# Optimization experiments

Measured on AMD Instinct MI355X. Metric: run time of the kernel, lower is better.

Reference implementation:

```python
import jax, jax.numpy as jnp
import numpy as np
from jax import lax

# SLAYER neuron / simulation constants (from netParams)
THETA = 10.0       # spike threshold
TAU_SR = 10.0      # synaptic (PSP) time constant
TAU_REF = 1.0      # refractory time constant
SCALE_REF = 2.0    # refractory scale
TAU_RHO = 1.0      # surrogate-gradient width (unused in fwd)
K_PSP = 32         # truncation length of SRM alpha kernel
K_REF = 16         # truncation length of refractory kernel

_t = np.arange(K_PSP, dtype=np.float64)
PSP_KERN = jnp.asarray((_t / TAU_SR) * np.exp(1.0 - _t / TAU_SR), jnp.float32)  # [K_PSP]
_tr = np.arange(1, K_REF + 1, dtype=np.float64)
REF_KERN = jnp.asarray(-SCALE_REF * THETA * (_tr / TAU_REF) * np.exp(1.0 - _tr / TAU_REF), jnp.float32)  # [K_REF]


def psp(x):
    """Causal temporal FIR filter with SRM alpha kernel; x: [..., T]."""
    sh = x.shape
    T = sh[-1]
    flat = x.reshape(-1, 1, T)                       # [B*, 1, T]
    k = PSP_KERN[::-1][None, None, :]                # correlation kernel (reversed)
    y = lax.conv_general_dilated(flat, k, (1,), [(K_PSP - 1, 0)])
    return y.reshape(sh)


def spike(u):
    """Threshold with refractory feedback, sequential over time. u: [..., T]."""
    uT = jnp.moveaxis(u, -1, 0)                      # [T, ...]
    buf0 = jnp.zeros(u.shape[:-1] + (K_REF,), u.dtype)

    def step(buf, ut):
        v = ut + buf[..., 0]
        s = (v >= THETA).astype(u.dtype)
        buf = jnp.concatenate([buf[..., 1:], jnp.zeros_like(buf[..., :1])], -1)
        buf = buf + s[..., None] * REF_KERN
        return buf, s

    _, sT = lax.scan(step, buf0, uT)
    return jnp.moveaxis(sT, 0, -1)


def conv_t(x, w, stride, pad):
    """2D conv applied independently per timestep. x: [N,C,H,W,T], w: [Co,C,kh,kw]."""
    N, C, H, W, T = x.shape
    xt = jnp.moveaxis(x, -1, 1).reshape(N * T, C, H, W)
    y = lax.conv_general_dilated(xt, w, (stride, stride), [(pad, pad), (pad, pad)])
    Co, Ho, Wo = y.shape[1], y.shape[2], y.shape[3]
    return jnp.moveaxis(y.reshape(N, T, Co, Ho, Wo), 1, -1)


def pool_t(x):
    """SLAYER sum-pool 2x2/s2 with weight 1.1*theta/kernel_area. x: [N,C,H,W,T]."""
    s = lax.reduce_window(x, np.float32(0.0), lax.add, (1, 1, 2, 2, 1), (1, 1, 2, 2, 1), 'VALID')
    return s * np.float32(1.1 * THETA / 4.0)


def setup_inputs() -> dict:
    key = jax.random.key(0)
    ks = jax.random.split(key, 5)
    spikeInput = (jax.random.uniform(ks[0], (4, 2, 256, 256, 50)) < 0.02).astype(jnp.float32)
    w1 = jax.random.normal(ks[1], (8, 2, 5, 5), jnp.float32) * 2.0
    w2 = jax.random.normal(ks[2], (16, 8, 3, 3), jnp.float32) * 1.5
    w3 = jax.random.normal(ks[3], (32, 16, 3, 3), jnp.float32) * 1.5
    w_fc = jax.random.normal(ks[4], (2, 32, 8, 8), jnp.float32) * 0.3
    return {"spikeInput": spikeInput, "w1": w1, "w2": w2, "w3": w3, "w_fc": w_fc}


def reference(spikeInput, w1, w2, w3, w_fc):
    x = spike(conv_t(psp(spikeInput), w1, 2, 1))   # [4,8,127,127,50]
    x = spike(pool_t(psp(x)))                      # [4,8,63,63,50]
    x = spike(conv_t(psp(x), w2, 2, 1))            # [4,16,32,32,50]
    x = spike(pool_t(psp(x)))                      # [4,16,16,16,50]
    x = spike(conv_t(psp(x), w3, 2, 1))            # [4,32,8,8,50]
    u = psp(x)
    out = jnp.einsum('ochw,nchwt->not', w_fc, u)   # dense over (C,H,W)
    return spike(out[:, :, None, None, :])         # [4,2,1,1,50]
```

## Files before the change

### kernel.cpp

```cpp
#include <hip/hip_runtime.h>
#include <cmath>

struct K32 { float k[32]; };
struct K16 { float k[16]; };

#define THETA 10.0f

__global__ __launch_bounds__(128)
void psp_kernel(const float* __restrict__ in, float* __restrict__ out,
                int nrows, K32 pk) {
  __shared__ __align__(16) float lds[64 * 50];
  const int rowBase = blockIdx.x * 64;
  const int tid = threadIdx.x;
  const int vr = min(64, nrows - rowBase);
  const int n4 = (vr * 50) >> 2;
  const float4* g4 = (const float4*)(in + (size_t)rowBase * 50);
  for (int i = tid; i < n4; i += 128) *(float4*)(&lds[4 * i]) = g4[i];
  __syncthreads();
  const int r = tid & 63;
  const int part = tid >> 6;
  const bool act = r < vr;
  float x[50];
  if (act) {
    if (part == 0) {
#pragma unroll
      for (int t = 0; t < 25; ++t) x[t] = lds[r * 50 + t];
    } else {
#pragma unroll
      for (int t = 0; t < 50; ++t) x[t] = lds[r * 50 + t];
    }
  }
  __syncthreads();
  if (act) {
    if (part == 0) {
#pragma unroll
      for (int t = 0; t < 25; ++t) {
        float a = 0.f;
#pragma unroll
        for (int k = 31; k >= 0; --k)
          if (t - k >= 0) a += x[t - k] * pk.k[k];
        lds[r * 50 + t] = a;
      }
    } else {
#pragma unroll
      for (int t = 25; t < 50; ++t) {
        float a = 0.f;
#pragma unroll
        for (int k = 31; k >= 0; --k)
          if (t - k >= 0) a += x[t - k] * pk.k[k];
        lds[r * 50 + t] = a;
      }
    }
  }
  __syncthreads();
  float4* o4 = (float4*)(out + (size_t)rowBase * 50);
  for (int i = tid; i < n4; i += 128) o4[i] = *(const float4*)(&lds[4 * i]);
}

template <int CIN, int COUT, int KK, int HIN, int WIN, int S1H, int S1W,
          int S2H, int S2W>
__global__ __launch_bounds__(256)
void conv_pps_kernel(const float* __restrict__ x, const float* __restrict__ w,
                     float* __restrict__ s2out, K32 pk, K16 rk) {
  constexpr int WT = 4;
  constexpr int SW = 8;
  constexpr int XR = 2 * (WT - 1) + KK;
  constexpr int GROUPS = (S1W + SW - 1) / SW;
  constexpr int NROW = COUT * 2 * SW;
  __shared__ float lds[NROW * 51];
  const int tid = threadIdx.x;
  const int wave = tid >> 6;
  const int lane = tid & 63;
  const int group = blockIdx.x % GROUPS;
  const int rest = blockIdx.x / GROUPS;
  const int hop = rest % S2H;
  const int n = rest / S2H;
  const int ho_off = wave & 1;
  const int wo_half = wave >> 1;
  const int ho = 2 * hop + ho_off;
  const int wo0 = group * SW + wo_half * WT;
  const int tt = lane < 50 ? lane : 49;

  float acc[COUT][WT] = {};
  for (int c = 0; c < CIN; ++c) {
#pragma unroll
    for (int kh = 0; kh < KK; ++kh) {
      const int hi = 2 * ho + kh - 1;
      if ((unsigned)hi >= (unsigned)HIN) continue;
      float xr[XR];
#pragma unroll
      for (int i = 0; i < XR; ++i) {
        const int wi = 2 * wo0 - 1 + i;
        xr[i] = ((unsigned)wi < (unsigned)WIN)
                    ? x[(((size_t)(n * CIN + c) * HIN + hi) * WIN + wi) * 50 + tt]
                    : 0.f;
      }
#pragma unroll
      for (int co = 0; co < COUT; ++co)
#pragma unroll
        for (int kw = 0; kw < KK; ++kw) {
          const float wv = w[((co * CIN + c) * KK + kh) * KK + kw];
#pragma unroll
          for (int wl = 0; wl < WT; ++wl)
            acc[co][wl] += xr[2 * wl + kw] * wv;
        }
    }
  }
  if (lane < 50) {
#pragma unroll
    for (int co = 0; co < COUT; ++co)
#pragma unroll
      for (int wl = 0; wl < WT; ++wl)
        lds[((co * 2 + ho_off) * SW + wo_half * WT + wl) * 51 + lane] = acc[co][wl];
  }
  __syncthreads();
  if (tid < NROW) {
    const int wol = tid & (SW - 1);
    if (group * SW + wol < S1W) {
      float buf[16];
#pragma unroll
      for (int j = 0; j < 16; ++j) buf[j] = 0.f;
#pragma unroll
      for (int t = 0; t < 50; ++t) {
        float v = lds[tid * 51 + t] + buf[t & 15];
        buf[t & 15] = 0.f;
        float sp = 0.f;
        if (v >= THETA) {
          sp = 1.f;
#pragma unroll
          for (int j = 0; j < 16; ++j) buf[(t + 1 + j) & 15] += rk.k[j];
        }
        lds[tid * 51 + t] = sp;
      }
    }
  }
  __syncthreads();
  {
    const int r = tid & (NROW - 1);
    const int part = tid >> 7;
    const int wol = r & (SW - 1);
    const bool act = (group * SW + wol) < S1W;
    float xs[50];
    if (act) {
      if (part == 0) {
#pragma unroll
        for (int t = 0; t < 25; ++t) xs[t] = lds[r * 51 + t];
      } else {
#pragma unroll
        for (int t = 0; t < 50; ++t) xs[t] = lds[r * 51 + t];
      }
    }
    __syncthreads();
    if (act) {
      if (part == 0) {
#pragma unroll
        for (int t = 0; t < 25; ++t) {
          float a = 0.f;
#pragma unroll
          for (int k = 31; k >= 0; --k)
            if (t - k >= 0) a += xs[t - k] * pk.k[k];
          lds[r * 51 + t] = a;
        }
      } else {
#pragma unroll
        for (int t = 25; t < 50; ++t) {
          float a = 0.f;
#pragma unroll
          for (int k = 31; k >= 0; --k)
            if (t - k >= 0) a += xs[t - k] * pk.k[k];
          lds[r * 51 + t] = a;
        }
      }
    }
  }
  __syncthreads();
  if (tid < COUT * (SW / 2)) {
    const int co = tid / (SW / 2);
    const int wpl = tid % (SW / 2);
    const int wop = group * (SW / 2) + wpl;
    if (wop < S2W) {
      const int r00 = (co * 16 + 2 * wpl) * 51;
      const int r01 = (co * 16 + 2 * wpl + 1) * 51;
      const int r10 = (co * 16 + 8 + 2 * wpl) * 51;
      const int r11 = (co * 16 + 8 + 2 * wpl + 1) * 51;
      float* orow = s2out + (((size_t)(n * COUT + co) * S2H + hop) * S2W + wop) * 50;
      float buf[16];
#pragma unroll
      for (int j = 0; j < 16; ++j) buf[j] = 0.f;
      float prev = 0.f;
#pragma unroll
      for (int t = 0; t < 50; ++t) {
        const float u0 = (((lds[r00 + t] + lds[r01 + t]) + lds[r10 + t]) + lds[r11 + t]) * 2.75f;
        float v = u0 + buf[t & 15];
        buf[t & 15] = 0.f;
        float sp = 0.f;
        if (v >= THETA) {
          sp = 1.f;
#pragma unroll
          for (int j = 0; j < 16; ++j) buf[(t + 1 + j) & 15] += rk.k[j];
        }
        if (t & 1) *(float2*)(orow + t - 1) = make_float2(prev, sp);
        else prev = sp;
      }
    }
  }
}

template <int CIN, int COUT, int KK, int WT, int HIN, int WIN, int HOUT, int WOUT>
__global__ __launch_bounds__(256)
void conv_spike_kernel(const float* __restrict__ x, const float* __restrict__ w,
                       float* __restrict__ s, K16 rk) {
  constexpr int XR = 2 * (WT - 1) + KK;
  constexpr int TW = 4 * WT;
  constexpr int GROUPS = (WOUT + TW - 1) / TW;
  __shared__ float lds[COUT * TW * 51];
  const int tid = threadIdx.x;
  const int wave = tid >> 6;
  const int lane = tid & 63;
  const int group = blockIdx.x % GROUPS;
  const int rest = blockIdx.x / GROUPS;
  const int ho = rest % HOUT;
  const int n = rest / HOUT;
  const int wo0 = group * TW + wave * WT;
  const int tt = lane < 50 ? lane : 49;

  float acc[COUT][WT] = {};
  for (int c = 0; c < CIN; ++c) {
#pragma unroll
    for (int kh = 0; kh < KK; ++kh) {
      const int hi = 2 * ho + kh - 1;
      if ((unsigned)hi >= (unsigned)HIN) continue;
      float xr[XR];
#pragma unroll
      for (int i = 0; i < XR; ++i) {
        const int wi = 2 * wo0 - 1 + i;
        xr[i] = ((unsigned)wi < (unsigned)WIN)
                    ? x[(((size_t)(n * CIN + c) * HIN + hi) * WIN + wi) * 50 + tt]
                    : 0.f;
      }
#pragma unroll
      for (int co = 0; co < COUT; ++co)
#pragma unroll
        for (int kw = 0; kw < KK; ++kw) {
          const float wv = w[((co * CIN + c) * KK + kh) * KK + kw];
#pragma unroll
          for (int wl = 0; wl < WT; ++wl)
            acc[co][wl] += xr[2 * wl + kw] * wv;
        }
    }
  }

  if (lane < 50) {
#pragma unroll
    for (int co = 0; co < COUT; ++co)
#pragma unroll
      for (int wl = 0; wl < WT; ++wl)
        lds[(co * TW + wave * WT + wl) * 51 + lane] = acc[co][wl];
  }
  __syncthreads();
  if (tid < COUT * TW) {
    const int co = tid / TW;
    const int wol = tid - co * TW;
    const int wo = group * TW + wol;
    if (wo < WOUT) {
      float* orow = s + (((size_t)(n * COUT + co) * HOUT + ho) * WOUT + wo) * 50;
      float buf[16];
#pragma unroll
      for (int j = 0; j < 16; ++j) buf[j] = 0.f;
      float prev = 0.f;
#pragma unroll
      for (int t = 0; t < 50; ++t) {
        float v = lds[tid * 51 + t] + buf[t & 15];
        buf[t & 15] = 0.f;
        float sp = 0.f;
        if (v >= THETA) {
          sp = 1.f;
#pragma unroll
          for (int j = 0; j < 16; ++j) buf[(t + 1 + j) & 15] += rk.k[j];
        }
        if (t & 1) *(float2*)(orow + t - 1) = make_float2(prev, sp);
        else prev = sp;
      }
    }
  }
}

__global__ __launch_bounds__(128)
void pps_kernel(const float* __restrict__ in, float* __restrict__ out,
                int Hin, int Win, int Hout, int Wout, int nseg,
                K32 pk, K16 rk) {
  __shared__ __align__(16) float lds[80 * 50];
  const int tid = threadIdx.x;
  const int seg = blockIdx.x % nseg;
  const int rest = blockIdx.x / nseg;
  const int ho = rest % Hout;
  const int nc = rest / Hout;
  const int wbase = seg * 32;
  const int nw = min(32, 2 * Wout - wbase);
  const int nwo = nw >> 1;
  const int span = nw * 50;
  const float* b0 = in + ((size_t)(nc * Hin + 2 * ho) * Win + wbase) * 50;
  const float* b1 = b0 + (size_t)Win * 50;
  const int n2 = span >> 1;
  for (int i = tid; i < n2; i += 128) {
    *(float2*)(&lds[2 * i]) = *(const float2*)(b0 + 2 * i);
    *(float2*)(&lds[span + 2 * i]) = *(const float2*)(b1 + 2 * i);
  }
  __syncthreads();
  const int r = tid & 63;
  const int part = tid >> 6;
  const bool act = r < 2 * nw;
  float x[50];
  if (act) {
    if (part == 0) {
#pragma unroll
      for (int t = 0; t < 25; ++t) x[t] = lds[r * 50 + t];
    } else {
#pragma unroll
      for (int t = 0; t < 50; ++t) x[t] = lds[r * 50 + t];
    }
  }
  __syncthreads();
  if (act) {
    if (part == 0) {
#pragma unroll
      for (int t = 0; t < 25; ++t) {
        float a = 0.f;
#pragma unroll
        for (int k = 31; k >= 0; --k)
          if (t - k >= 0) a += x[t - k] * pk.k[k];
        lds[r * 50 + t] = a;
      }
    } else {
#pragma unroll
      for (int t = 25; t < 50; ++t) {
        float a = 0.f;
#pragma unroll
        for (int k = 31; k >= 0; --k)
          if (t - k >= 0) a += x[t - k] * pk.k[k];
        lds[r * 50 + t] = a;
      }
    }
  }
  __syncthreads();
  if (tid < nwo) {
    float buf[16];
#pragma unroll
    for (int j = 0; j < 16; ++j) buf[j] = 0.f;
    const int r00 = (2 * tid) * 50, r01 = (2 * tid + 1) * 50;
    const int r10 = (nw + 2 * tid) * 50, r11 = (nw + 2 * tid + 1) * 50;
    const int ro = (2 * nw + tid) * 50;
#pragma unroll
    for (int t = 0; t < 50; ++t) {
      const float u0 = (((lds[r00 + t] + lds[r01 + t]) + lds[r10 + t]) + lds[r11 + t]) * 2.75f;
      float v = u0 + buf[t & 15];
      buf[t & 15] = 0.f;
      float sp = 0.f;
      if (v >= THETA) {
        sp = 1.f;
#pragma unroll
        for (int j = 0; j < 16; ++j) buf[(t + 1 + j) & 15] += rk.k[j];
      }
      lds[ro + t] = sp;
    }
  }
  __syncthreads();
  float* ob = out + ((size_t)(nc * Hout + ho) * Wout + seg * 16) * 50;
  const int base = 2 * nw * 50;
  for (int i = tid; i < nwo * 25; i += 128)
    *(float2*)(ob + 2 * i) = *(const float2*)(&lds[base + 2 * i]);
}

__global__ __launch_bounds__(512)
void fc_spike_kernel(const float* __restrict__ w, const float* __restrict__ u,
                     float* __restrict__ out, K16 rk) {
  __shared__ float lds[8 * 51];
  const int tid = threadIdx.x;
  const int wave = tid >> 6, lane = tid & 63;
  const int o = wave & 1, n = wave >> 1;
  const int tt = lane < 50 ? lane : 49;
  const float* wrow = w + (size_t)o * 2048;
  const float* ub = u + (size_t)n * 2048 * 50;
  float acc = 0.f;
#pragma unroll 32
  for (int i = 0; i < 2048; ++i) acc += wrow[i] * ub[(size_t)i * 50 + tt];
  if (lane < 50) lds[wave * 51 + lane] = acc;
  __syncthreads();
  if (tid < 8) {
    float buf[16];
#pragma unroll
    for (int j = 0; j < 16; ++j) buf[j] = 0.f;
#pragma unroll
    for (int t = 0; t < 50; ++t) {
      float v = lds[tid * 51 + t] + buf[t & 15];
      buf[t & 15] = 0.f;
      float sp = 0.f;
      if (v >= THETA) {
        sp = 1.f;
#pragma unroll
        for (int j = 0; j < 16; ++j) buf[(t + 1 + j) & 15] += rk.k[j];
      }
      out[tid * 50 + t] = sp;
    }
  }
}

extern "C" void kernel_launch(void* const* d_in, const int* in_sizes, int n_in,
                              void* d_out, int out_size, void* d_ws, size_t ws_size,
                              hipStream_t stream) {
  const float* xin = (const float*)d_in[0];
  const float* w1  = (const float*)d_in[1];
  const float* w2  = (const float*)d_in[2];
  const float* w3  = (const float*)d_in[3];
  const float* wfc = (const float*)d_in[4];
  float* out = (float*)d_out;

  float* R0 = (float*)d_ws;
  float* R1 = R0 + 26214400;

  K32 pk;
  for (int k = 0; k < 32; ++k)
    pk.k[k] = (float)(((double)k / 10.0) * exp(1.0 - (double)k / 10.0));
  K16 rk;
  for (int j = 0; j < 16; ++j) {
    const double tr = (double)(j + 1);
    rk.k[j] = (float)(-2.0 * 10.0 * tr * exp(1.0 - tr));
  }

  psp_kernel<<<8192, 128, 0, stream>>>(xin, R0, 524288, pk);
  conv_pps_kernel<2, 8, 5, 256, 256, 127, 127, 63, 63>
      <<<4 * 63 * 16, 256, 0, stream>>>(R0, w1, R1, pk, rk);
  psp_kernel<<<1985, 128, 0, stream>>>(R1, R0, 127008, pk);
  conv_spike_kernel<8, 16, 3, 1, 63, 63, 32, 32>
      <<<4 * 32 * 8, 256, 0, stream>>>(R0, w2, R1, rk);
  pps_kernel<<<4 * 16 * 16, 128, 0, stream>>>(R1, R0, 32, 32, 16, 16, 1, pk, rk);
  psp_kernel<<<256, 128, 0, stream>>>(R0, R1, 16384, pk);
  conv_spike_kernel<16, 32, 3, 1, 16, 16, 8, 8>
      <<<4 * 8 * 2, 256, 0, stream>>>(R1, w3, R0, rk);
  psp_kernel<<<128, 128, 0, stream>>>(R0, R1, 8192, pk);
  fc_spike_kernel<<<1, 512, 0, stream>>>(wfc, R1, out, rk);
}
```

Baseline: 505.6 us.

## Commute PSP filter past linear conv, pool and FC stages and fuse into them

The temporal PSP filter is linear and acts per pixel, so it commutes with the per-timestep spatial convolutions, sum-pooling and the dense FC layer. Each PSP is therefore applied after the spatial op, inside the conv, pool and FC kernels, and all standalone psp_kernel launches are removed. This drops several full global-memory round trips, including the large filtered copy of the input, and cuts the launch count. In return each fused kernel does extra in-LDS FIR work, sometimes on more rows than before. The changed float summation order can flip spikes that sit right at the threshold.

```diff
diff --git a/kernel.cpp b/kernel.cpp
--- a/kernel.cpp
+++ b/kernel.cpp
@@ -5,57 +5,6 @@
 struct K16 { float k[16]; };
 
 #define THETA 10.0f
-
-__global__ __launch_bounds__(128)
-void psp_kernel(const float* __restrict__ in, float* __restrict__ out,
-                int nrows, K32 pk) {
-  __shared__ __align__(16) float lds[64 * 50];
-  const int rowBase = blockIdx.x * 64;
-  const int tid = threadIdx.x;
-  const int vr = min(64, nrows - rowBase);
-  const int n4 = (vr * 50) >> 2;
-  const float4* g4 = (const float4*)(in + (size_t)rowBase * 50);
-  for (int i = tid; i < n4; i += 128) *(float4*)(&lds[4 * i]) = g4[i];
-  __syncthreads();
-  const int r = tid & 63;
-  const int part = tid >> 6;
-  const bool act = r < vr;
-  float x[50];
-  if (act) {
-    if (part == 0) {
-#pragma unroll
-      for (int t = 0; t < 25; ++t) x[t] = lds[r * 50 + t];
-    } else {
-#pragma unroll
-      for (int t = 0; t < 50; ++t) x[t] = lds[r * 50 + t];
-    }
-  }
-  __syncthreads();
-  if (act) {
-    if (part == 0) {
-#pragma unroll
-      for (int t = 0; t < 25; ++t) {
-        float a = 0.f;
-#pragma unroll
-        for (int k = 31; k >= 0; --k)
-          if (t - k >= 0) a += x[t - k] * pk.k[k];
-        lds[r * 50 + t] = a;
-      }
-    } else {
-#pragma unroll
-      for (int t = 25; t < 50; ++t) {
-        float a = 0.f;
-#pragma unroll
-        for (int k = 31; k >= 0; --k)
-          if (t - k >= 0) a += x[t - k] * pk.k[k];
-        lds[r * 50 + t] = a;
-      }
-    }
-  }
-  __syncthreads();
-  float4* o4 = (float4*)(out + (size_t)rowBase * 50);
-  for (int i = tid; i < n4; i += 128) o4[i] = *(const float4*)(&lds[4 * i]);
-}
 
 template <int CIN, int COUT, int KK, int HIN, int WIN, int S1H, int S1W,
           int S2H, int S2W>
@@ -114,6 +63,45 @@
         lds[((co * 2 + ho_off) * SW + wo_half * WT + wl) * 51 + lane] = acc[co][wl];
   }
   __syncthreads();
+  {
+    const int r = tid & (NROW - 1);
+    const int part = tid >> 7;
+    const int wol = r & (SW - 1);
+    const bool act = (group * SW + wol) < S1W;
+    float xs[50];
+    if (act) {
+      if (part == 0) {
+#pragma unroll
+        for (int t = 0; t < 25; ++t) xs[t] = lds[r * 51 + t];
+      } else {
+#pragma unroll
+        for (int t = 0; t < 50; ++t) xs[t] = lds[r * 51 + t];
+      }
+    }
+    __syncthreads();
+    if (act) {
+      if (part == 0) {
+#pragma unroll
+        for (int t = 0; t < 25; ++t) {
+          float a = 0.f;
+#pragma unroll
+          for (int k = 31; k >= 0; --k)
+            if (t - k >= 0) a += xs[t - k] * pk.k[k];
+          lds[r * 51 + t] = a;
+        }
+      } else {
+#pragma unroll
+        for (int t = 25; t < 50; ++t) {
+          float a = 0.f;
+#pragma unroll
+          for (int k = 31; k >= 0; --k)
+            if (t - k >= 0) a += xs[t - k] * pk.k[k];
+          lds[r * 51 + t] = a;
+        }
+      }
+    }
+  }
+  __syncthreads();
   if (tid < NROW) {
     const int wol = tid & (SW - 1);
     if (group * SW + wol < S1W) {
@@ -136,18 +124,25 @@
   }
   __syncthreads();
   {
-    const int r = tid & (NROW - 1);
-    const int part = tid >> 7;
-    const int wol = r & (SW - 1);
-    const bool act = (group * SW + wol) < S1W;
+    const int r = tid & 31;
+    const int part = tid >> 5;
+    const int co = r >> 2;
+    const int wpl = r & 3;
+    const bool act = (part < 2) && (group * (SW / 2) + wpl < S2W);
+    const int r00 = (co * 16 + 2 * wpl) * 51;
+    const int r01 = r00 + 51;
+    const int r10 = (co * 16 + 8 + 2 * wpl) * 51;
+    const int r11 = r10 + 51;
     float xs[50];
     if (act) {
       if (part == 0) {
 #pragma unroll
-        for (int t = 0; t < 25; ++t) xs[t] = lds[r * 51 + t];
-      } else {
-#pragma unroll
-        for (int t = 0; t < 50; ++t) xs[t] = lds[r * 51 + t];
+        for (int t = 0; t < 25; ++t)
+          xs[t] = (((lds[r00 + t] + lds[r01 + t]) + lds[r10 + t]) + lds[r11 + t]) * 2.75f;
+      } else {
+#pragma unroll
+        for (int t = 0; t < 50; ++t)
+          xs[t] = (((lds[r00 + t] + lds[r01 + t]) + lds[r10 + t]) + lds[r11 + t]) * 2.75f;
       }
     }
     __syncthreads();
@@ -159,7 +154,7 @@
 #pragma unroll
           for (int k = 31; k >= 0; --k)
             if (t - k >= 0) a += xs[t - k] * pk.k[k];
-          lds[r * 51 + t] = a;
+          lds[r00 + t] = a;
         }
       } else {
 #pragma unroll
@@ -168,7 +163,7 @@
 #pragma unroll
           for (int k = 31; k >= 0; --k)
             if (t - k >= 0) a += xs[t - k] * pk.k[k];
-          lds[r * 51 + t] = a;
+          lds[r00 + t] = a;
         }
       }
     }
@@ -179,10 +174,7 @@
     const int wpl = tid % (SW / 2);
     const int wop = group * (SW / 2) + wpl;
     if (wop < S2W) {
-      const int r00 = (co * 16 + 2 * wpl) * 51;
-      const int r01 = (co * 16 + 2 * wpl + 1) * 51;
-      const int r10 = (co * 16 + 8 + 2 * wpl) * 51;
-      const int r11 = (co * 16 + 8 + 2 * wpl + 1) * 51;
+      const int rr = (co * 16 + 2 * wpl) * 51;
       float* orow = s2out + (((size_t)(n * COUT + co) * S2H + hop) * S2W + wop) * 50;
       float buf[16];
 #pragma unroll
@@ -190,8 +182,7 @@
       float prev = 0.f;
 #pragma unroll
       for (int t = 0; t < 50; ++t) {
-        const float u0 = (((lds[r00 + t] + lds[r01 + t]) + lds[r10 + t]) + lds[r11 + t]) * 2.75f;
-        float v = u0 + buf[t & 15];
+        float v = lds[rr + t] + buf[t & 15];
         buf[t & 15] = 0.f;
         float sp = 0.f;
         if (v >= THETA) {
@@ -208,12 +199,13 @@
 
 template <int CIN, int COUT, int KK, int WT, int HIN, int WIN, int HOUT, int WOUT>
 __global__ __launch_bounds__(256)
-void conv_spike_kernel(const float* __restrict__ x, const float* __restrict__ w,
-                       float* __restrict__ s, K16 rk) {
+void conv_fir_spike_kernel(const float* __restrict__ x, const float* __restrict__ w,
+                           float* __restrict__ s, K32 pk, K16 rk) {
   constexpr int XR = 2 * (WT - 1) + KK;
   constexpr int TW = 4 * WT;
   constexpr int GROUPS = (WOUT + TW - 1) / TW;
-  __shared__ float lds[COUT * TW * 51];
+  constexpr int NROW = COUT * TW;
+  __shared__ float lds[NROW * 51];
   const int tid = threadIdx.x;
   const int wave = tid >> 6;
   const int lane = tid & 63;
@@ -258,7 +250,46 @@
         lds[(co * TW + wave * WT + wl) * 51 + lane] = acc[co][wl];
   }
   __syncthreads();
-  if (tid < COUT * TW) {
+  {
+    const int r = tid % NROW;
+    const int part = tid / NROW;
+    const int wol = r % TW;
+    const bool act = (part < 2) && (group * TW + wol < WOUT);
+    float xs[50];
+    if (act) {
+      if (part == 0) {
+#pragma unroll
+        for (int t = 0; t < 25; ++t) xs[t] = lds[r * 51 + t];
+      } else {
+#pragma unroll
+        for (int t = 0; t < 50; ++t) xs[t] = lds[r * 51 + t];
+      }
+    }
+    __syncthreads();
+    if (act) {
+      if (part == 0) {
+#pragma unroll
+        for (int t = 0; t < 25; ++t) {
+          float a = 0.f;
+#pragma unroll
+          for (int k = 31; k >= 0; --k)
+            if (t - k >= 0) a += xs[t - k] * pk.k[k];
+          lds[r * 51 + t] = a;
+        }
+      } else {
+#pragma unroll
+        for (int t = 25; t < 50; ++t) {
+          float a = 0.f;
+#pragma unroll
+          for (int k = 31; k >= 0; --k)
+            if (t - k >= 0) a += xs[t - k] * pk.k[k];
+          lds[r * 51 + t] = a;
+        }
+      }
+    }
+  }
+  __syncthreads();
+  if (tid < NROW) {
     const int co = tid / TW;
     const int wol = tid - co * TW;
     const int wo = group * TW + wol;
@@ -286,74 +317,64 @@
 }
 
 __global__ __launch_bounds__(128)
-void pps_kernel(const float* __restrict__ in, float* __restrict__ out,
-                int Hin, int Win, int Hout, int Wout, int nseg,
-                K32 pk, K16 rk) {
-  __shared__ __align__(16) float lds[80 * 50];
+void pool_fir_spike_kernel(const float* __restrict__ in, float* __restrict__ out,
+                           int Hin, int Win, int Hout, int Wout, K32 pk, K16 rk) {
+  __shared__ __align__(16) float lds[64 * 50 + 16 * 50];
   const int tid = threadIdx.x;
-  const int seg = blockIdx.x % nseg;
-  const int rest = blockIdx.x / nseg;
-  const int ho = rest % Hout;
-  const int nc = rest / Hout;
-  const int wbase = seg * 32;
-  const int nw = min(32, 2 * Wout - wbase);
-  const int nwo = nw >> 1;
-  const int span = nw * 50;
-  const float* b0 = in + ((size_t)(nc * Hin + 2 * ho) * Win + wbase) * 50;
-  const float* b1 = b0 + (size_t)Win * 50;
-  const int n2 = span >> 1;
-  for (int i = tid; i < n2; i += 128) {
-    *(float2*)(&lds[2 * i]) = *(const float2*)(b0 + 2 * i);
-    *(float2*)(&lds[span + 2 * i]) = *(const float2*)(b1 + 2 * i);
-  }
-  __syncthreads();
-  const int r = tid & 63;
-  const int part = tid >> 6;
-  const bool act = r < 2 * nw;
-  float x[50];
-  if (act) {
-    if (part == 0) {
-#pragma unroll
-      for (int t = 0; t < 25; ++t) x[t] = lds[r * 50 + t];
-    } else {
-#pragma unroll
-      for (int t = 0; t < 50; ++t) x[t] = lds[r * 50 + t];
-    }
-  }
-  __syncthreads();
-  if (act) {
-    if (part == 0) {
-#pragma unroll
-      for (int t = 0; t < 25; ++t) {
-        float a = 0.f;
-#pragma unroll
-        for (int k = 31; k >= 0; --k)
-          if (t - k >= 0) a += x[t - k] * pk.k[k];
-        lds[r * 50 + t] = a;
-      }
-    } else {
-#pragma unroll
-      for (int t = 25; t < 50; ++t) {
-        float a = 0.f;
-#pragma unroll
-        for (int k = 31; k >= 0; --k)
-          if (t - k >= 0) a += x[t - k] * pk.k[k];
-        lds[r * 50 + t] = a;
-      }
-    }
-  }
-  __syncthreads();
-  if (tid < nwo) {
+  const int ho = blockIdx.x % Hout;
+  const int nc = blockIdx.x / Hout;
+  const float* b0 = in + ((size_t)(nc * Hin + 2 * ho) * Win) * 50;
+  const int n4 = (2 * Win * 50) >> 2;
+  const float4* g4 = (const float4*)b0;
+  for (int i = tid; i < n4; i += 128) *(float4*)(&lds[4 * i]) = g4[i];
+  __syncthreads();
+  {
+    const int r = tid & 15;
+    const int part = tid >> 4;
+    const bool act = (part < 2) && (r < Wout);
+    const int c00 = (2 * r) * 50, c01 = c00 + 50;
+    const int c10 = Win * 50 + c00, c11 = Win * 50 + c01;
+    const int ro = 64 * 50 + r * 50;
+    float xs[50];
+    if (act) {
+      if (part == 0) {
+#pragma unroll
+        for (int t = 0; t < 25; ++t)
+          xs[t] = (((lds[c00 + t] + lds[c01 + t]) + lds[c10 + t]) + lds[c11 + t]) * 2.75f;
+#pragma unroll
+        for (int t = 0; t < 25; ++t) {
+          float a = 0.f;
+#pragma unroll
+          for (int k = 31; k >= 0; --k)
+            if (t - k >= 0) a += xs[t - k] * pk.k[k];
+          lds[ro + t] = a;
+        }
+      } else {
+#pragma unroll
+        for (int t = 0; t < 50; ++t)
+          xs[t] = (((lds[c00 + t] + lds[c01 + t]) + lds[c10 + t]) + lds[c11 + t]) * 2.75f;
+#pragma unroll
+        for (int t = 25; t < 50; ++t) {
+          float a = 0.f;
+#pragma unroll
+          for (int k = 31; k >= 0; --k)
+            if (t - k >= 0) a += xs[t - k] * pk.k[k];
+          lds[ro + t] = a;
+        }
+      }
+    }
+  }
+  __syncthreads();
+  if (tid < 16 && tid < Wout) {
+    const int ro = 64 * 50 + tid * 50;
+    float* orow = out + (((size_t)nc * Hout + ho) * Wout + tid) * 50;
     float buf[16];
 #pragma unroll
     for (int j = 0; j < 16; ++j) buf[j] = 0.f;
-    const int r00 = (2 * tid) * 50, r01 = (2 * tid + 1) * 50;
-    const int r10 = (nw + 2 * tid) * 50, r11 = (nw + 2 * tid + 1) * 50;
-    const int ro = (2 * nw + tid) * 50;
+    float prev = 0.f;
 #pragma unroll
     for (int t = 0; t < 50; ++t) {
-      const float u0 = (((lds[r00 + t] + lds[r01 + t]) + lds[r10 + t]) + lds[r11 + t]) * 2.75f;
-      float v = u0 + buf[t & 15];
+      float v = lds[ro + t] + buf[t & 15];
       buf[t & 15] = 0.f;
       float sp = 0.f;
       if (v >= THETA) {
@@ -361,30 +382,64 @@
 #pragma unroll
         for (int j = 0; j < 16; ++j) buf[(t + 1 + j) & 15] += rk.k[j];
       }
-      lds[ro + t] = sp;
-    }
-  }
-  __syncthreads();
-  float* ob = out + ((size_t)(nc * Hout + ho) * Wout + seg * 16) * 50;
-  const int base = 2 * nw * 50;
-  for (int i = tid; i < nwo * 25; i += 128)
-    *(float2*)(ob + 2 * i) = *(const float2*)(&lds[base + 2 * i]);
+      if (t & 1) *(float2*)(orow + t - 1) = make_float2(prev, sp);
+      else prev = sp;
+    }
+  }
 }
 
 __global__ __launch_bounds__(512)
-void fc_spike_kernel(const float* __restrict__ w, const float* __restrict__ u,
-                     float* __restrict__ out, K16 rk) {
+void fc_fir_spike_kernel(const float* __restrict__ w, const float* __restrict__ s,
+                         float* __restrict__ out, K32 pk, K16 rk) {
   __shared__ float lds[8 * 51];
   const int tid = threadIdx.x;
   const int wave = tid >> 6, lane = tid & 63;
   const int o = wave & 1, n = wave >> 1;
   const int tt = lane < 50 ? lane : 49;
   const float* wrow = w + (size_t)o * 2048;
-  const float* ub = u + (size_t)n * 2048 * 50;
+  const float* ub = s + (size_t)n * 2048 * 50;
   float acc = 0.f;
 #pragma unroll 32
   for (int i = 0; i < 2048; ++i) acc += wrow[i] * ub[(size_t)i * 50 + tt];
   if (lane < 50) lds[wave * 51 + lane] = acc;
+  __syncthreads();
+  {
+    const int r = tid & 7;
+    const int part = tid >> 3;
+    const bool act = part < 2;
+    float xs[50];
+    if (act) {
+      if (part == 0) {
+#pragma unroll
+        for (int t = 0; t < 25; ++t) xs[t] = lds[r * 51 + t];
+      } else {
+#pragma unroll
+        for (int t = 0; t < 50; ++t) xs[t] = lds[r * 51 + t];
+      }
+    }
+    __syncthreads();
+    if (act) {
+      if (part == 0) {
+#pragma unroll
+        for (int t = 0; t < 25; ++t) {
+          float a = 0.f;
+#pragma unroll
+          for (int k = 31; k >= 0; --k)
+            if (t - k >= 0) a += xs[t - k] * pk.k[k];
+          lds[r * 51 + t] = a;
+        }
+      } else {
+#pragma unroll
+        for (int t = 25; t < 50; ++t) {
+          float a = 0.f;
+#pragma unroll
+          for (int k = 31; k >= 0; --k)
+            if (t - k >= 0) a += xs[t - k] * pk.k[k];
+          lds[r * 51 + t] = a;
+        }
+      }
+    }
+  }
   __syncthreads();
   if (tid < 8) {
     float buf[16];
@@ -427,16 +482,12 @@
     rk.k[j] = (float)(-2.0 * 10.0 * tr * exp(1.0 - tr));
   }
 
-  psp_kernel<<<8192, 128, 0, stream>>>(xin, R0, 524288, pk);
   conv_pps_kernel<2, 8, 5, 256, 256, 127, 127, 63, 63>
-      <<<4 * 63 * 16, 256, 0, stream>>>(R0, w1, R1, pk, rk);
-  psp_kernel<<<1985, 128, 0, stream>>>(R1, R0, 127008, pk);
-  conv_spike_kernel<8, 16, 3, 1, 63, 63, 32, 32>
-      <<<4 * 32 * 8, 256, 0, stream>>>(R0, w2, R1, rk);
-  pps_kernel<<<4 * 16 * 16, 128, 0, stream>>>(R1, R0, 32, 32, 16, 16, 1, pk, rk);
-  psp_kernel<<<256, 128, 0, stream>>>(R0, R1, 16384, pk);
-  conv_spike_kernel<16, 32, 3, 1, 16, 16, 8, 8>
-      <<<4 * 8 * 2, 256, 0, stream>>>(R1, w3, R0, rk);
-  psp_kernel<<<128, 128, 0, stream>>>(R0, R1, 8192, pk);
-  fc_spike_kernel<<<1, 512, 0, stream>>>(wfc, R1, out, rk);
+      <<<4 * 63 * 16, 256, 0, stream>>>(xin, w1, R0, pk, rk);
+  conv_fir_spike_kernel<8, 16, 3, 1, 63, 63, 32, 32>
+      <<<4 * 32 * 8, 256, 0, stream>>>(R0, w2, R1, pk, rk);
+  pool_fir_spike_kernel<<<4 * 16 * 16, 128, 0, stream>>>(R1, R0, 32, 32, 16, 16, pk, rk);
+  conv_fir_spike_kernel<16, 32, 3, 1, 16, 16, 8, 8>
+      <<<4 * 8 * 2, 256, 0, stream>>>(R0, w3, R1, pk, rk);
+  fc_fir_spike_kernel<<<1, 512, 0, stream>>>(wfc, R1, out, pk, rk);
 }
```

Result: slower. 583.7 us (+15.4%).
